# Optimization experiments

Measured on AMD Instinct MI355X. Metric: run time of the kernel, lower is better.

The kernel has to match this reference:

```python
import jax, jax.numpy as jnp
import numpy as np
from math import sqrt

DIM = 256
HEADS = 4
GROUPS = min(DIM // 4, 32)  # = 32
EPS = 1e-6


def setup_inputs() -> dict:
    key = jax.random.key(0)
    ks = jax.random.split(key, 10)
    B, C, H, W = 16, DIM, 32, 32
    x = jax.random.normal(ks[0], (B, C, H, W), dtype=jnp.float32)
    s = 1.0 / sqrt(C)
    inp = {
        'x': x,
        'gn_scale': jnp.ones((C,), jnp.float32),
        'gn_bias': jnp.zeros((C,), jnp.float32),
        'Wq': jax.random.normal(ks[1], (C, C), jnp.float32) * s,
        'bq': jnp.zeros((C,), jnp.float32),
        'Wk': jax.random.normal(ks[2], (C, C), jnp.float32) * s,
        'bk': jnp.zeros((C,), jnp.float32),
        'Wv': jax.random.normal(ks[3], (C, C), jnp.float32) * s,
        'bv': jnp.zeros((C,), jnp.float32),
        'Wp': jax.random.normal(ks[4], (C, C), jnp.float32) * s,
        'bp': jnp.zeros((C,), jnp.float32),
    }
    return inp


def _group_norm(x, scale, bias):
    B, C, H, W = x.shape
    xg = x.reshape(B, GROUPS, C // GROUPS, H, W)
    mean = xg.mean(axis=(2, 3, 4), keepdims=True)
    var = xg.var(axis=(2, 3, 4), keepdims=True)
    xg = (xg - mean) * jax.lax.rsqrt(var + EPS)
    x = xg.reshape(B, C, H, W)
    return x * scale[None, :, None, None] + bias[None, :, None, None]


def _lin_ch(x, W, b):
    # 1x1 conv / linear over channel dim: (B,C,H,W) x (C,Cout) -> (B,Cout,H,W)
    return jnp.einsum('bchw,cd->bdhw', x, W) + b[None, :, None, None]


def reference(x, gn_scale, gn_bias, Wq, bq, Wk, bk, Wv, bv, Wp, bp):
    B, C, H, W = x.shape
    dh = C // HEADS
    _x = _group_norm(x, gn_scale, gn_bias)
    q = _lin_ch(_x, Wq, bq).reshape(B, HEADS, dh, H, W)
    k = _lin_ch(_x, Wk, bk).reshape(B, HEADS, dh, H, W)
    v = _lin_ch(_x, Wv, bv).reshape(B, HEADS, dh, H, W)
    scores = jnp.einsum('bhdxy,bhdij->bhxyij', q, k) / sqrt(C)
    scores = scores.reshape(B, HEADS, H, W, H * W)
    weights = jax.nn.softmax(scores, axis=-1).reshape(B, HEADS, H, W, H, W)
    h = jnp.einsum('bhxyij,bhdij->bhdxy', weights, v).reshape(B, C, H, W)
    h = _lin_ch(h, Wp, bp)
    ret = (x + h) / sqrt(2.0)
    return ret
```

## Files before the change

kernel.cpp:

```cpp
#include <hip/hip_runtime.h>
#include <hip/hip_bf16.h>

#define BATCH 16
#define CH    256
#define HW    1024
#define NH    4
#define DH    64
#define NG    32
#define CPG   8
#define EPSV  1e-6f

#define QSCALE 0.090168440055558706f

typedef __bf16 bf16x8 __attribute__((ext_vector_type(8)));
typedef float  f32x4  __attribute__((ext_vector_type(4)));

__device__ __forceinline__ unsigned short f2bf(float f) {
    union { __hip_bfloat16 h; unsigned short u; } cv;
    cv.h = __float2bfloat16(f);
    return cv.u;
}

__device__ __forceinline__ unsigned int fbits(float f) {
    union { float f; unsigned int u; } cv; cv.f = f; return cv.u;
}

__device__ __forceinline__ void gld_lds16(const unsigned short* g, unsigned short* l) {
    __builtin_amdgcn_global_load_lds(
        (const __attribute__((address_space(1))) void*)g,
        (__attribute__((address_space(3))) void*)l, 16, 0, 0);
}

__global__ void prep_kernel(const float* Wq, const float* Wk, const float* Wv,
                            const float* Wp, const float* bq, const float* bk,
                            const float* bv, unsigned short* wqkv_t,
                            unsigned short* wp_t, float* bqkv) {
    int idx = blockIdx.x * 256 + threadIdx.x;
    if (idx < 768 * 256) {
        int n = idx >> 8, c = idx & 255;
        const float* W = (n < 256) ? Wq : (n < 512) ? Wk : Wv;
        int d = n & 255;
        wqkv_t[idx] = f2bf(W[c * 256 + d]);
    } else if (idx < 768 * 256 + 256 * 256) {
        int j = idx - 768 * 256;
        int n = j >> 8, c = j & 255;
        wp_t[j] = f2bf(Wp[c * 256 + n]);
    }
    if (idx < 768)
        bqkv[idx] = (idx < 256) ? bq[idx] : (idx < 512) ? bk[idx - 256] : bv[idx - 512];
}

__global__ void gn_stats_kernel(const float* x, const float* scale, const float* bias,
                                float* coefA, float* coefB) {
    int bg = blockIdx.x;
    const float4* p = reinterpret_cast<const float4*>(x + (size_t)bg * (CPG * HW));
    int t = threadIdx.x;
    float s = 0.f, ss = 0.f;
    for (int i = t; i < CPG * HW / 4; i += 256) {
        float4 v = p[i];
        s += v.x + v.y + v.z + v.w;
        ss += v.x * v.x + v.y * v.y + v.z * v.z + v.w * v.w;
    }
    for (int o = 32; o; o >>= 1) { s += __shfl_down(s, o); ss += __shfl_down(ss, o); }
    __shared__ float as[4], ass[4];
    int w = t >> 6;
    if ((t & 63) == 0) { as[w] = s; ass[w] = ss; }
    __syncthreads();
    if (t < 8) {
        float S = as[0] + as[1] + as[2] + as[3];
        float SS = ass[0] + ass[1] + ass[2] + ass[3];
        float mean = S / (float)(CPG * HW);
        float var = SS / (float)(CPG * HW) - mean * mean;
        float rstd = rsqrtf(var + EPSV);
        int b = bg >> 5, g = bg & 31;
        int c = g * CPG + t;
        float a = rstd * scale[c];
        coefA[b * CH + c] = a;
        coefB[b * CH + c] = bias[c] - mean * a;
    }
}

__global__ __launch_bounds__(256) void qkv_kernel(const float* x,
        const float* coefA, const float* coefB,
        const unsigned short* wqkv_t, const float* bqkv,
        unsigned short* qb, unsigned short* kb, unsigned short* vb) {
    int t = threadIdx.x;
    int wv = t >> 6, lane = t & 63, quad = lane >> 4, ln = lane & 15;
    int wr = wv >> 1, wc = wv & 1;
    int bx = blockIdx.x;
    int m0 = bx * 128 + wr * 64;
    int n0 = blockIdx.y * 128 + wc * 64;
    int bb = bx >> 3;
    int p0 = (bx & 7) * 128;

    __shared__ __align__(16) unsigned short lds_a[128][40];

    const float* xb = x + (size_t)bb * CH * HW + p0;
    const float* cA = coefA + bb * CH;
    const float* cB = coefB + bb * CH;

    int sp = t & 127;
    int sbase = (t >> 7) * 2;

    f32x4 acc[4][4] = {};
    for (int k0 = 0; k0 < CH; k0 += 32) {
        bf16x8 wpk[2];
#pragma unroll
        for (int rep = 0; rep < 2; rep++) {
            int s = sbase + rep;
            int cb = k0 + s * 8;
            union { bf16x8 v8; __hip_bfloat162 h2[4]; } u;
#pragma unroll
            for (int j = 0; j < 4; j++) {
                float v0 = fmaf(xb[(size_t)(cb + 2 * j)     * HW + sp], cA[cb + 2 * j],     cB[cb + 2 * j]);
                float v1 = fmaf(xb[(size_t)(cb + 2 * j + 1) * HW + sp], cA[cb + 2 * j + 1], cB[cb + 2 * j + 1]);
                u.h2[j] = __float22bfloat162_rn(float2{v0, v1});
            }
            wpk[rep] = u.v8;
        }
        __syncthreads();
#pragma unroll
        for (int rep = 0; rep < 2; rep++) {
            int s = sbase + rep;
            int phys = s ^ (sp & 3);
            *reinterpret_cast<bf16x8*>(&lds_a[sp][phys * 8]) = wpk[rep];
        }
        __syncthreads();
        bf16x8 af[4], bfr[4];
#pragma unroll
        for (int i = 0; i < 4; i++) {
            int p = wr * 64 + i * 16 + ln;
            af[i] = *reinterpret_cast<const bf16x8*>(&lds_a[p][(quad ^ (p & 3)) * 8]);
        }
#pragma unroll
        for (int j = 0; j < 4; j++)
            bfr[j] = *reinterpret_cast<const bf16x8*>(
                wqkv_t + (size_t)(n0 + j * 16 + ln) * CH + k0 + quad * 8);
#pragma unroll
        for (int i = 0; i < 4; i++)
#pragma unroll
            for (int j = 0; j < 4; j++)
                acc[i][j] = __builtin_amdgcn_mfma_f32_16x16x32_bf16(af[i], bfr[j], acc[i][j], 0, 0, 0);
    }
#pragma unroll
    for (int j = 0; j < 4; j++) {
        int n = n0 + j * 16 + ln;
        float bias = bqkv[n];
        int which = n >> 8;
        int dh_ = n & 255;
        int head = dh_ >> 6, d = dh_ & 63;
#pragma unroll
        for (int i = 0; i < 4; i++) {
            int mb = m0 + i * 16 + quad * 4;
            int bi = mb >> 10, p = mb & 1023;
            int bh = bi * NH + head;
            if (which < 2) {
                unsigned short* dst = (which == 0 ? qb : kb) + (size_t)bh * HW * DH;
                float sc = (which == 0) ? QSCALE : 1.0f;
#pragma unroll
                for (int r = 0; r < 4; r++)
                    dst[(size_t)(p + r) * DH + d] = f2bf((acc[i][j][r] + bias) * sc);
            } else {
                unsigned short* dst = vb + ((size_t)bh * DH + d) * HW + p;
                ushort4 pk4;
                pk4.x = f2bf(acc[i][j][0] + bias);
                pk4.y = f2bf(acc[i][j][1] + bias);
                pk4.z = f2bf(acc[i][j][2] + bias);
                pk4.w = f2bf(acc[i][j][3] + bias);
                *reinterpret_cast<ushort4*>(dst) = pk4;
            }
        }
    }
}

__global__ __launch_bounds__(256) void attn_kernel(const unsigned short* qb,
        const unsigned short* kb, const unsigned short* vb, unsigned short* h_t) {
    int qblk = blockIdx.x, bh = blockIdx.y;
    int t = threadIdx.x;
    int wv = t >> 6, lane = t & 63, quad = lane >> 4, ln = lane & 15;
    int q0 = qblk * 128 + wv * 32;

    const unsigned short* Q = qb + (size_t)bh * HW * DH;
    const unsigned short* K = kb + (size_t)bh * HW * DH;
    const unsigned short* V = vb + (size_t)bh * DH * HW;

    __shared__ __align__(16) unsigned short kbuf[2][4096];
    __shared__ __align__(16) unsigned short vbuf[2][4096];
    __shared__ __align__(16) unsigned short pbuf[4][2][16][72];

    int c_a = wv * 64 + lane;
    int c_b = 256 + wv * 64 + lane;
    int pa = c_a >> 3, ja = (c_a & 7) ^ (pa & 7);
    int pb = c_b >> 3, jb = (c_b & 7) ^ (pb & 7);
    const unsigned short* pka = K + (size_t)pa * DH + ja * 8;
    const unsigned short* pkb = K + (size_t)pb * DH + jb * 8;
    const unsigned short* pva = V + (size_t)pa * HW + ja * 8;
    const unsigned short* pvb = V + (size_t)pb * HW + jb * 8;
    int lofs_a = wv * 512, lofs_b = 2048 + wv * 512;

    int koffs[4][2];
#pragma unroll
    for (int mt = 0; mt < 4; mt++) {
        int p = mt * 16 + ln, sw = p & 7;
#pragma unroll
        for (int kk = 0; kk < 2; kk++)
            koffs[mt][kk] = p * 64 + (((kk * 4 + quad) ^ sw) * 8);
    }

    bf16x8 qf[2][2];
#pragma unroll
    for (int nq = 0; nq < 2; nq++)
#pragma unroll
        for (int kk = 0; kk < 2; kk++)
            qf[nq][kk] = *reinterpret_cast<const bf16x8*>(
                Q + (size_t)(q0 + nq * 16 + ln) * DH + kk * 32 + quad * 8);

    f32x4 ls[2] = {};
    f32x4 o[2][4] = {};

    gld_lds16(pka, &kbuf[0][lofs_a]);
    gld_lds16(pkb, &kbuf[0][lofs_b]);
    gld_lds16(pva, &vbuf[0][lofs_a]);
    gld_lds16(pvb, &vbuf[0][lofs_b]);
    pka += 64 * DH; pkb += 64 * DH; pva += 64; pvb += 64;

#define ATTN_TILE(B, DO_STAGE)                                                      \
    {                                                                               \
        __syncthreads();                                                            \
        if (DO_STAGE) {                                                             \
            gld_lds16(pka, &kbuf[B ^ 1][lofs_a]);                                   \
            gld_lds16(pkb, &kbuf[B ^ 1][lofs_b]);                                   \
            gld_lds16(pva, &vbuf[B ^ 1][lofs_a]);                                   \
            gld_lds16(pvb, &vbuf[B ^ 1][lofs_b]);                                   \
            pka += 64 * DH; pkb += 64 * DH; pva += 64; pvb += 64;                   \
        }                                                                           \
        bf16x8 kf[4][2], vf[4][2];                                                  \
        _Pragma("unroll")                                                           \
        for (int mt = 0; mt < 4; mt++) {                                            \
            _Pragma("unroll")                                                       \
            for (int kk = 0; kk < 2; kk++) {                                        \
                kf[mt][kk] = *reinterpret_cast<const bf16x8*>(&kbuf[B][koffs[mt][kk]]); \
                vf[mt][kk] = *reinterpret_cast<const bf16x8*>(&vbuf[B][koffs[mt][kk]]); \
            }                                                                       \
        }                                                                           \
        f32x4 s[2][4] = {};                                                         \
        _Pragma("unroll")                                                           \
        for (int nq = 0; nq < 2; nq++)                                              \
            _Pragma("unroll")                                                       \
            for (int mt = 0; mt < 4; mt++) {                                        \
                s[nq][mt] = __builtin_amdgcn_mfma_f32_16x16x32_bf16(kf[mt][0], qf[nq][0], s[nq][mt], 0, 0, 0); \
                s[nq][mt] = __builtin_amdgcn_mfma_f32_16x16x32_bf16(kf[mt][1], qf[nq][1], s[nq][mt], 0, 0, 0); \
            }                                                                       \
        _Pragma("unroll")                                                           \
        for (int nq = 0; nq < 2; nq++)                                              \
            _Pragma("unroll")                                                       \
            for (int mt = 0; mt < 4; mt++) {                                        \
                float e0 = __builtin_amdgcn_exp2f(s[nq][mt][0]);                    \
                float e1 = __builtin_amdgcn_exp2f(s[nq][mt][1]);                    \
                float e2 = __builtin_amdgcn_exp2f(s[nq][mt][2]);                    \
                float e3 = __builtin_amdgcn_exp2f(s[nq][mt][3]);                    \
                ls[nq][0] += e0; ls[nq][1] += e1;                                   \
                ls[nq][2] += e2; ls[nq][3] += e3;                                   \
                uint2 pk2;                                                          \
                pk2.x = __builtin_amdgcn_perm(fbits(e1), fbits(e0), 0x07060302u);   \
                pk2.y = __builtin_amdgcn_perm(fbits(e3), fbits(e2), 0x07060302u);   \
                *reinterpret_cast<uint2*>(&pbuf[wv][nq][ln][mt * 16 + quad * 4]) = pk2; \
            }                                                                       \
        _Pragma("unroll")                                                           \
        for (int nq = 0; nq < 2; nq++)                                              \
            _Pragma("unroll")                                                       \
            for (int kk = 0; kk < 2; kk++) {                                        \
                bf16x8 pf = *reinterpret_cast<const bf16x8*>(&pbuf[wv][nq][ln][kk * 32 + quad * 8]); \
                _Pragma("unroll")                                                   \
                for (int mt = 0; mt < 4; mt++)                                      \
                    o[nq][mt] = __builtin_amdgcn_mfma_f32_16x16x32_bf16(vf[mt][kk], pf, o[nq][mt], 0, 0, 0); \
            }                                                                       \
    }

    for (int u = 0; u < 8; u++) {
        ATTN_TILE(0, true)
        ATTN_TILE(1, (u < 7))
    }
#undef ATTN_TILE

    int b_ = bh >> 2, head = bh & 3;
#pragma unroll
    for (int nq = 0; nq < 2; nq++) {
        float lsum = ls[nq][0] + ls[nq][1] + ls[nq][2] + ls[nq][3];
        lsum += __shfl_xor(lsum, 16);
        lsum += __shfl_xor(lsum, 32);
        float inv = 1.0f / lsum;
        unsigned short* dst = h_t + ((size_t)b_ * HW + q0 + nq * 16 + ln) * CH + head * DH;
#pragma unroll
        for (int mt = 0; mt < 4; mt++) {
            ushort4 pk4;
            pk4.x = f2bf(o[nq][mt][0] * inv);
            pk4.y = f2bf(o[nq][mt][1] * inv);
            pk4.z = f2bf(o[nq][mt][2] * inv);
            pk4.w = f2bf(o[nq][mt][3] * inv);
            *reinterpret_cast<ushort4*>(dst + mt * 16 + quad * 4) = pk4;
        }
    }
}

__global__ __launch_bounds__(256) void proj_kernel(const unsigned short* h_t,
        const unsigned short* wp_t, const float* bp, const float* x, float* out) {
    int t = threadIdx.x;
    int wv = t >> 6, lane = t & 63, quad = lane >> 4, ln = lane & 15;
    int wr = wv >> 1, wc = wv & 1;
    int m0 = blockIdx.x * 64 + wr * 32;
    int n0 = blockIdx.y * 128 + wc * 64;

    f32x4 acc[2][4] = {};
    for (int k0 = 0; k0 < CH; k0 += 32) {
        int koff = k0 + quad * 8;
        bf16x8 af[2], bfr[4];
#pragma unroll
        for (int i = 0; i < 2; i++)
            af[i] = *reinterpret_cast<const bf16x8*>(h_t + (size_t)(m0 + i * 16 + ln) * CH + koff);
#pragma unroll
        for (int j = 0; j < 4; j++)
            bfr[j] = *reinterpret_cast<const bf16x8*>(wp_t + (size_t)(n0 + j * 16 + ln) * CH + koff);
#pragma unroll
        for (int i = 0; i < 2; i++)
#pragma unroll
            for (int j = 0; j < 4; j++)
                acc[i][j] = __builtin_amdgcn_mfma_f32_16x16x32_bf16(af[i], bfr[j], acc[i][j], 0, 0, 0);
    }
    const float inv_s2 = 0.70710678118654752440f;
#pragma unroll
    for (int j = 0; j < 4; j++) {
        int n = n0 + j * 16 + ln;
        float bias = bp[n];
#pragma unroll
        for (int i = 0; i < 2; i++) {
            int mb = m0 + i * 16 + quad * 4;
            int bi = mb >> 10, p = mb & 1023;
            size_t off = ((size_t)(bi * CH + n)) * HW + p;
            float4 xv = *reinterpret_cast<const float4*>(x + off);
            float4 ov;
            ov.x = (xv.x + acc[i][j][0] + bias) * inv_s2;
            ov.y = (xv.y + acc[i][j][1] + bias) * inv_s2;
            ov.z = (xv.z + acc[i][j][2] + bias) * inv_s2;
            ov.w = (xv.w + acc[i][j][3] + bias) * inv_s2;
            *reinterpret_cast<float4*>(out + off) = ov;
        }
    }
}

extern "C" void kernel_launch(void* const* d_in, const int* in_sizes, int n_in,
                              void* d_out, int out_size, void* d_ws, size_t ws_size,
                              hipStream_t stream) {
    const float* x        = (const float*)d_in[0];
    const float* gn_scale = (const float*)d_in[1];
    const float* gn_bias  = (const float*)d_in[2];
    const float* Wq = (const float*)d_in[3];
    const float* bq = (const float*)d_in[4];
    const float* Wk = (const float*)d_in[5];
    const float* bk = (const float*)d_in[6];
    const float* Wv = (const float*)d_in[7];
    const float* bv = (const float*)d_in[8];
    const float* Wp = (const float*)d_in[9];
    const float* bp = (const float*)d_in[10];
    float* out = (float*)d_out;

    char* ws = (char*)d_ws;
    float*          bqkv   = (float*)(ws + 0);
    float*          coefA  = (float*)(ws + 4096);
    float*          coefB  = (float*)(ws + 20480);
    unsigned short* wqkv_t = (unsigned short*)(ws + 36864);
    unsigned short* wp_t   = (unsigned short*)(ws + 430080);
    unsigned short* h_t    = (unsigned short*)(ws + 1048576);
    unsigned short* qb     = (unsigned short*)(ws + 9437184);
    unsigned short* kb     = (unsigned short*)(ws + 17825792);
    unsigned short* vb     = (unsigned short*)(ws + 26214400);

    prep_kernel<<<1024, 256, 0, stream>>>(Wq, Wk, Wv, Wp, bq, bk, bv, wqkv_t, wp_t, bqkv);
    gn_stats_kernel<<<512, 256, 0, stream>>>(x, gn_scale, gn_bias, coefA, coefB);
    qkv_kernel<<<dim3(128, 6), 256, 0, stream>>>(x, coefA, coefB, wqkv_t, bqkv, qb, kb, vb);
    attn_kernel<<<dim3(8, 64), 256, 0, stream>>>(qb, kb, vb, h_t);
    proj_kernel<<<dim3(256, 2), 256, 0, stream>>>(h_t, wp_t, bp, x, out);
}
```

Measured before the change: 162.3 us.

## Merge prep and stats kernels, stage Q/K epilogue through LDS, retile projection

Folds the weight-conversion prep kernel and the group-norm stats kernel into one launch, which removes one kernel launch. The Q/K epilogue in the QKV kernel now goes through a per-wave LDS buffer, so each thread writes 16-byte contiguous bf16 rows instead of scattered 2-byte stores. The attention grid is flattened so blocks that share the same query tile but come from different batch-heads are scheduled next to each other. The projection kernel is retiled to 16-row blocks with each wave covering 64 output columns, giving more, smaller blocks. The costs are extra LDS use and occupancy pressure in the QKV kernel, and reloading the full Wp once per small block in the projection.

```diff
diff --git a/kernel.cpp b/kernel.cpp
--- a/kernel.cpp
+++ b/kernel.cpp
@@ -31,30 +31,31 @@
         (__attribute__((address_space(3))) void*)l, 16, 0, 0);
 }
 
-__global__ void prep_kernel(const float* Wq, const float* Wk, const float* Wv,
-                            const float* Wp, const float* bq, const float* bk,
-                            const float* bv, unsigned short* wqkv_t,
-                            unsigned short* wp_t, float* bqkv) {
-    int idx = blockIdx.x * 256 + threadIdx.x;
-    if (idx < 768 * 256) {
-        int n = idx >> 8, c = idx & 255;
-        const float* W = (n < 256) ? Wq : (n < 512) ? Wk : Wv;
-        int d = n & 255;
-        wqkv_t[idx] = f2bf(W[c * 256 + d]);
-    } else if (idx < 768 * 256 + 256 * 256) {
-        int j = idx - 768 * 256;
-        int n = j >> 8, c = j & 255;
-        wp_t[j] = f2bf(Wp[c * 256 + n]);
-    }
-    if (idx < 768)
-        bqkv[idx] = (idx < 256) ? bq[idx] : (idx < 512) ? bk[idx - 256] : bv[idx - 512];
-}
-
-__global__ void gn_stats_kernel(const float* x, const float* scale, const float* bias,
-                                float* coefA, float* coefB) {
+__global__ void prep_stats_kernel(const float* x, const float* scale, const float* bias,
+                                  const float* Wq, const float* Wk, const float* Wv,
+                                  const float* Wp, const float* bq, const float* bk,
+                                  const float* bv, float* coefA, float* coefB,
+                                  unsigned short* wqkv_t, unsigned short* wp_t,
+                                  float* bqkv) {
+    int t = threadIdx.x;
+    if (blockIdx.x >= 512) {
+        int idx = (blockIdx.x - 512) * 256 + t;
+        if (idx < 768 * 256) {
+            int n = idx >> 8, c = idx & 255;
+            const float* W = (n < 256) ? Wq : (n < 512) ? Wk : Wv;
+            int d = n & 255;
+            wqkv_t[idx] = f2bf(W[c * 256 + d]);
+        } else if (idx < 768 * 256 + 256 * 256) {
+            int j = idx - 768 * 256;
+            int n = j >> 8, c = j & 255;
+            wp_t[j] = f2bf(Wp[c * 256 + n]);
+        }
+        if (idx < 768)
+            bqkv[idx] = (idx < 256) ? bq[idx] : (idx < 512) ? bk[idx - 256] : bv[idx - 512];
+        return;
+    }
     int bg = blockIdx.x;
     const float4* p = reinterpret_cast<const float4*>(x + (size_t)bg * (CPG * HW));
-    int t = threadIdx.x;
     float s = 0.f, ss = 0.f;
     for (int i = t; i < CPG * HW / 4; i += 256) {
         float4 v = p[i];
@@ -94,6 +95,7 @@
     int p0 = (bx & 7) * 128;
 
     __shared__ __align__(16) unsigned short lds_a[128][40];
+    __shared__ __align__(16) float ebuf[4][16][68];
 
     const float* xb = x + (size_t)bb * CH * HW + p0;
     const float* cA = coefA + bb * CH;
@@ -142,32 +144,55 @@
             for (int j = 0; j < 4; j++)
                 acc[i][j] = __builtin_amdgcn_mfma_f32_16x16x32_bf16(af[i], bfr[j], acc[i][j], 0, 0, 0);
     }
-#pragma unroll
-    for (int j = 0; j < 4; j++) {
-        int n = n0 + j * 16 + ln;
-        float bias = bqkv[n];
-        int which = n >> 8;
-        int dh_ = n & 255;
-        int head = dh_ >> 6, d = dh_ & 63;
+
+    int whichw = n0 >> 8;
+    int headw = (n0 >> 6) & 3;
+    int bi = m0 >> 10;
+    int p0w = m0 & 1023;
+    int bh = bi * NH + headw;
+    float biasj[4];
+#pragma unroll
+    for (int j = 0; j < 4; j++) biasj[j] = bqkv[n0 + j * 16 + ln];
+
+    if (whichw < 2) {
+        unsigned short* dst = (whichw == 0 ? qb : kb) + (size_t)bh * HW * DH;
+        float sc = (whichw == 0) ? QSCALE : 1.0f;
 #pragma unroll
         for (int i = 0; i < 4; i++) {
-            int mb = m0 + i * 16 + quad * 4;
-            int bi = mb >> 10, p = mb & 1023;
-            int bh = bi * NH + head;
-            if (which < 2) {
-                unsigned short* dst = (which == 0 ? qb : kb) + (size_t)bh * HW * DH;
-                float sc = (which == 0) ? QSCALE : 1.0f;
+#pragma unroll
+            for (int j = 0; j < 4; j++)
 #pragma unroll
                 for (int r = 0; r < 4; r++)
-                    dst[(size_t)(p + r) * DH + d] = f2bf((acc[i][j][r] + bias) * sc);
-            } else {
-                unsigned short* dst = vb + ((size_t)bh * DH + d) * HW + p;
+                    ebuf[wv][quad * 4 + r][j * 16 + ln] = (acc[i][j][r] + biasj[j]) * sc;
+#pragma unroll
+            for (int pg = 0; pg < 2; pg++) {
+                int mloc = pg * 8 + quad * 2 + (ln >> 3);
+                int dd = (ln & 7) * 8;
+                f32x4 a0 = *reinterpret_cast<const f32x4*>(&ebuf[wv][mloc][dd]);
+                f32x4 a1 = *reinterpret_cast<const f32x4*>(&ebuf[wv][mloc][dd + 4]);
+                union { uint4 u4; unsigned int u[4]; } o;
+                union { __hip_bfloat162 h2; unsigned int u; } cv;
+                cv.h2 = __float22bfloat162_rn(float2{a0[0], a0[1]}); o.u[0] = cv.u;
+                cv.h2 = __float22bfloat162_rn(float2{a0[2], a0[3]}); o.u[1] = cv.u;
+                cv.h2 = __float22bfloat162_rn(float2{a1[0], a1[1]}); o.u[2] = cv.u;
+                cv.h2 = __float22bfloat162_rn(float2{a1[2], a1[3]}); o.u[3] = cv.u;
+                *reinterpret_cast<uint4*>(dst + (size_t)(p0w + i * 16 + mloc) * DH + dd) = o.u4;
+            }
+        }
+    } else {
+        unsigned short* dstv = vb + (size_t)bh * DH * HW;
+#pragma unroll
+        for (int j = 0; j < 4; j++) {
+            int d = j * 16 + ln;
+#pragma unroll
+            for (int i = 0; i < 4; i++) {
+                int p = p0w + i * 16 + quad * 4;
                 ushort4 pk4;
-                pk4.x = f2bf(acc[i][j][0] + bias);
-                pk4.y = f2bf(acc[i][j][1] + bias);
-                pk4.z = f2bf(acc[i][j][2] + bias);
-                pk4.w = f2bf(acc[i][j][3] + bias);
-                *reinterpret_cast<ushort4*>(dst) = pk4;
+                pk4.x = f2bf(acc[i][j][0] + biasj[j]);
+                pk4.y = f2bf(acc[i][j][1] + biasj[j]);
+                pk4.z = f2bf(acc[i][j][2] + biasj[j]);
+                pk4.w = f2bf(acc[i][j][3] + biasj[j]);
+                *reinterpret_cast<ushort4*>(dstv + (size_t)d * HW + p) = pk4;
             }
         }
     }
@@ -175,7 +200,9 @@
 
 __global__ __launch_bounds__(256) void attn_kernel(const unsigned short* qb,
         const unsigned short* kb, const unsigned short* vb, unsigned short* h_t) {
-    int qblk = blockIdx.x, bh = blockIdx.y;
+    int linear = blockIdx.x;
+    int bh = linear & 63;
+    int qblk = linear >> 6;
     int t = threadIdx.x;
     int wv = t >> 6, lane = t & 63, quad = lane >> 4, ln = lane & 15;
     int q0 = qblk * 128 + wv * 32;
@@ -307,44 +334,36 @@
         const unsigned short* wp_t, const float* bp, const float* x, float* out) {
     int t = threadIdx.x;
     int wv = t >> 6, lane = t & 63, quad = lane >> 4, ln = lane & 15;
-    int wr = wv >> 1, wc = wv & 1;
-    int m0 = blockIdx.x * 64 + wr * 32;
-    int n0 = blockIdx.y * 128 + wc * 64;
-
-    f32x4 acc[2][4] = {};
+    int m0 = blockIdx.x * 16;
+    int n0 = wv * 64;
+
+    f32x4 acc[4] = {};
     for (int k0 = 0; k0 < CH; k0 += 32) {
         int koff = k0 + quad * 8;
-        bf16x8 af[2], bfr[4];
-#pragma unroll
-        for (int i = 0; i < 2; i++)
-            af[i] = *reinterpret_cast<const bf16x8*>(h_t + (size_t)(m0 + i * 16 + ln) * CH + koff);
+        bf16x8 af = *reinterpret_cast<const bf16x8*>(h_t + (size_t)(m0 + ln) * CH + koff);
+        bf16x8 bfr[4];
 #pragma unroll
         for (int j = 0; j < 4; j++)
             bfr[j] = *reinterpret_cast<const bf16x8*>(wp_t + (size_t)(n0 + j * 16 + ln) * CH + koff);
 #pragma unroll
-        for (int i = 0; i < 2; i++)
-#pragma unroll
-            for (int j = 0; j < 4; j++)
-                acc[i][j] = __builtin_amdgcn_mfma_f32_16x16x32_bf16(af[i], bfr[j], acc[i][j], 0, 0, 0);
+        for (int j = 0; j < 4; j++)
+            acc[j] = __builtin_amdgcn_mfma_f32_16x16x32_bf16(af, bfr[j], acc[j], 0, 0, 0);
     }
     const float inv_s2 = 0.70710678118654752440f;
+    int mb = m0 + quad * 4;
+    int bi = mb >> 10, p = mb & 1023;
 #pragma unroll
     for (int j = 0; j < 4; j++) {
         int n = n0 + j * 16 + ln;
         float bias = bp[n];
-#pragma unroll
-        for (int i = 0; i < 2; i++) {
-            int mb = m0 + i * 16 + quad * 4;
-            int bi = mb >> 10, p = mb & 1023;
-            size_t off = ((size_t)(bi * CH + n)) * HW + p;
-            float4 xv = *reinterpret_cast<const float4*>(x + off);
-            float4 ov;
-            ov.x = (xv.x + acc[i][j][0] + bias) * inv_s2;
-            ov.y = (xv.y + acc[i][j][1] + bias) * inv_s2;
-            ov.z = (xv.z + acc[i][j][2] + bias) * inv_s2;
-            ov.w = (xv.w + acc[i][j][3] + bias) * inv_s2;
-            *reinterpret_cast<float4*>(out + off) = ov;
-        }
+        size_t off = ((size_t)(bi * CH + n)) * HW + p;
+        float4 xv = *reinterpret_cast<const float4*>(x + off);
+        float4 ov;
+        ov.x = (xv.x + acc[j][0] + bias) * inv_s2;
+        ov.y = (xv.y + acc[j][1] + bias) * inv_s2;
+        ov.z = (xv.z + acc[j][2] + bias) * inv_s2;
+        ov.w = (xv.w + acc[j][3] + bias) * inv_s2;
+        *reinterpret_cast<float4*>(out + off) = ov;
     }
 }
 
@@ -375,9 +394,9 @@
     unsigned short* kb     = (unsigned short*)(ws + 17825792);
     unsigned short* vb     = (unsigned short*)(ws + 26214400);
 
-    prep_kernel<<<1024, 256, 0, stream>>>(Wq, Wk, Wv, Wp, bq, bk, bv, wqkv_t, wp_t, bqkv);
-    gn_stats_kernel<<<512, 256, 0, stream>>>(x, gn_scale, gn_bias, coefA, coefB);
+    prep_stats_kernel<<<1536, 256, 0, stream>>>(x, gn_scale, gn_bias, Wq, Wk, Wv, Wp,
+                                                bq, bk, bv, coefA, coefB, wqkv_t, wp_t, bqkv);
     qkv_kernel<<<dim3(128, 6), 256, 0, stream>>>(x, coefA, coefB, wqkv_t, bqkv, qb, kb, vb);
-    attn_kernel<<<dim3(8, 64), 256, 0, stream>>>(qb, kb, vb, h_t);
-    proj_kernel<<<dim3(256, 2), 256, 0, stream>>>(h_t, wp_t, bp, x, out);
-}
+    attn_kernel<<<512, 256, 0, stream>>>(qb, kb, vb, h_t);
+    proj_kernel<<<dim3(1024, 1), 256, 0, stream>>>(h_t, wp_t, bp, x, out);
+}
```

Measured after the change: 162.7 us. Within noise of the previous version (+0.2%).
